# Optimization experiments

Hardware: AMD Instinct MI355X
Metric: run time of the kernel (lower is better)

## Reference

```python
import jax, jax.numpy as jnp
import numpy as np
import math

D_MODEL = 1024
NUM_HEADS = 16
B, L = 2, 2048
# scale_level=0, patch_time_span=1 -> effective_stride=1
PERIODS = (1.0, 30.0)
WEIGHTS = (0.8, 0.4)
SIGMAS = (0.5, 2.0)


def setup_inputs() -> dict:
    key = jax.random.key(0)
    ks = jax.random.split(key, 10)
    s = 1.0 / math.sqrt(D_MODEL)
    inp = {
        "x": jax.random.normal(ks[0], (B, L, D_MODEL), dtype=jnp.float32),
        "Wq": jax.random.normal(ks[1], (D_MODEL, D_MODEL), dtype=jnp.float32) * s,
        "bq": jax.random.normal(ks[2], (D_MODEL,), dtype=jnp.float32) * 0.01,
        "Wk": jax.random.normal(ks[3], (D_MODEL, D_MODEL), dtype=jnp.float32) * s,
        "bk": jax.random.normal(ks[4], (D_MODEL,), dtype=jnp.float32) * 0.01,
        "Wv": jax.random.normal(ks[5], (D_MODEL, D_MODEL), dtype=jnp.float32) * s,
        "bv": jax.random.normal(ks[6], (D_MODEL,), dtype=jnp.float32) * 0.01,
        "Wo": jax.random.normal(ks[7], (D_MODEL, D_MODEL), dtype=jnp.float32) * s,
        "bo": jax.random.normal(ks[8], (D_MODEL,), dtype=jnp.float32) * 0.01,
        "prior_lambda": jnp.asarray(2.0, dtype=jnp.float32),
    }
    return inp


def _gaussian_mask(length):
    idx = jnp.arange(length, dtype=jnp.float32)
    delta = jnp.abs(idx[:, None] - idx[None, :])  # [L, L]
    mask = jnp.zeros_like(delta)
    for p, w, sigma in zip(PERIODS, WEIGHTS, SIGMAS):
        if p < 0.2:
            continue
        mask = mask + w * jnp.exp(-((delta - p) ** 2) / (2.0 * sigma ** 2))
    return mask


def reference(x, Wq, bq, Wk, bk, Wv, bv, Wo, bo, prior_lambda):
    Bx, Lx, D = x.shape
    H = NUM_HEADS
    hd = D // H

    def split_heads(t):  # [B, L, D] -> [B, H, L, hd]
        return t.reshape(Bx, Lx, H, hd).transpose(0, 2, 1, 3)

    Q = split_heads(x @ Wq.T + bq)
    K = split_heads(x @ Wk.T + bk)
    V = split_heads(x @ Wv.T + bv)

    scores = jnp.einsum("bhqd,bhkd->bhqk", Q, K) / math.sqrt(hd)
    scores = scores + prior_lambda * _gaussian_mask(Lx)[None, None, :, :]
    attn = jax.nn.softmax(scores, axis=-1)
    out = jnp.einsum("bhqk,bhkd->bhqd", attn, V)
    out = out.transpose(0, 2, 1, 3).reshape(Bx, Lx, D)
    return out @ Wo.T + bo
```

## Files before the change

### kernel.cpp

```cpp
#include <hip/hip_runtime.h>

#define D_MODEL 1024
#define SEQ_L   2048
#define NHEADS  16
#define HDIM    64
#define NROWS   4096

typedef __attribute__((ext_vector_type(8))) short short8;
typedef __attribute__((ext_vector_type(4))) short short4v;
typedef __attribute__((ext_vector_type(4))) float floatx4;
typedef __attribute__((ext_vector_type(4))) unsigned short ushort4v;
typedef unsigned short ushort;

static __device__ __forceinline__ ushort f2bf(float f) {
    unsigned int u = __float_as_uint(f);
    u += 0x7FFFu + ((u >> 16) & 1u);
    return (ushort)(u >> 16);
}

static __device__ __forceinline__ floatx4 mfma16(short8 a, short8 b, floatx4 c) {
    return __builtin_amdgcn_mfma_f32_16x16x32_bf16(a, b, c, 0, 0, 0);
}

static __device__ __forceinline__ floatx4 mfma16k16(short4v a, short4v b, floatx4 c) {
    return __builtin_amdgcn_mfma_f32_16x16x16bf16_1k(a, b, c, 0, 0, 0);
}

static __device__ __forceinline__ void store8bf(ushort* dst, float4 a, float4 b) {
    uint4 pk;
    pk.x = (unsigned)f2bf(a.x) | ((unsigned)f2bf(a.y) << 16);
    pk.y = (unsigned)f2bf(a.z) | ((unsigned)f2bf(a.w) << 16);
    pk.z = (unsigned)f2bf(b.x) | ((unsigned)f2bf(b.y) << 16);
    pk.w = (unsigned)f2bf(b.z) | ((unsigned)f2bf(b.w) << 16);
    *(uint4*)dst = pk;
}

static __device__ __forceinline__ void gll16(const ushort* g, ushort* l) {
    __builtin_amdgcn_global_load_lds(
        (const __attribute__((address_space(1))) unsigned int*)(const unsigned int*)g,
        (__attribute__((address_space(3))) unsigned int*)(unsigned int*)l,
        16, 0, 0);
}

__global__ __launch_bounds__(256) void convert_bf16(
    const float* __restrict__ x,
    const float* __restrict__ wq, const float* __restrict__ wk,
    const float* __restrict__ wv, const float* __restrict__ wo,
    ushort* __restrict__ xb, ushort* __restrict__ wb3, ushort* __restrict__ wob)
{
    const int seg = blockIdx.y;
    const float* src;
    ushort* dst;
    int n;
    if      (seg == 0) { src = x;  dst = xb;                n = 4194304; }
    else if (seg == 1) { src = wq; dst = wb3;               n = 1048576; }
    else if (seg == 2) { src = wk; dst = wb3 + 1048576;     n = 1048576; }
    else if (seg == 3) { src = wv; dst = wb3 + 2097152;     n = 1048576; }
    else               { src = wo; dst = wob;               n = 1048576; }
    const int i = (blockIdx.x * 256 + threadIdx.x) * 8;
    if (i >= n) return;
    float4 a = *(const float4*)(src + i);
    float4 b = *(const float4*)(src + i + 4);
    store8bf(dst + i, a, b);
}

__global__ __launch_bounds__(256) void gemm_qkv(
    const ushort* __restrict__ A, const ushort* __restrict__ B,
    const float* __restrict__ bq, const float* __restrict__ bk,
    const float* __restrict__ bv,
    ushort* __restrict__ Qo, ushort* __restrict__ Ko, ushort* __restrict__ Vo)
{
    __shared__ ushort As[128 * 32];
    __shared__ ushort Bs[128 * 32];

    const int tid  = threadIdx.x;
    const int w    = tid >> 6;
    const int lane = tid & 63;
    const int l15  = lane & 15;
    const int quad = lane >> 4;
    const int wm   = w & 1;
    const int wn   = w >> 1;

    const int bm = blockIdx.y * 128;
    const int bn = blockIdx.x * 128;

    const int r0 = w * 16 + (lane >> 2);
    const int r1 = r0 + 64;
    const int c_ = lane & 3;
    const int g0 = c_ ^ ((r0 >> 1) & 3);
    const int g1 = c_ ^ ((r1 >> 1) & 3);

    const ushort* a0p = A + (size_t)(bm + r0) * 1024 + g0 * 8;
    const ushort* a1p = A + (size_t)(bm + r1) * 1024 + g1 * 8;
    const ushort* b0p = B + (size_t)(bn + r0) * 1024 + g0 * 8;
    const ushort* b1p = B + (size_t)(bn + r1) * 1024 + g1 * 8;
    ushort* lA0 = &As[r0 * 32 + c_ * 8];
    ushort* lA1 = &As[r1 * 32 + c_ * 8];
    ushort* lB0 = &Bs[r0 * 32 + c_ * 8];
    ushort* lB1 = &Bs[r1 * 32 + c_ * 8];

    const int cA = (quad ^ ((l15 >> 1) & 3)) * 8;

    floatx4 acc[4][4];
#pragma unroll
    for (int i = 0; i < 4; i++)
#pragma unroll
        for (int j = 0; j < 4; j++) acc[i][j] = (floatx4){0.f, 0.f, 0.f, 0.f};

    for (int k0 = 0; k0 < 1024; k0 += 32) {
        __syncthreads();
        gll16(a0p + k0, lA0);
        gll16(a1p + k0, lA1);
        gll16(b0p + k0, lB0);
        gll16(b1p + k0, lB1);
        __syncthreads();

        short8 af[4], bf[4];
#pragma unroll
        for (int mi = 0; mi < 4; mi++)
            af[mi] = *(const short8*)&As[(wm * 64 + mi * 16 + l15) * 32 + cA];
#pragma unroll
        for (int ni = 0; ni < 4; ni++)
            bf[ni] = *(const short8*)&Bs[(wn * 64 + ni * 16 + l15) * 32 + cA];
#pragma unroll
        for (int mi = 0; mi < 4; mi++)
#pragma unroll
            for (int ni = 0; ni < 4; ni++)
                acc[mi][ni] = mfma16(af[mi], bf[ni], acc[mi][ni]);
    }

#pragma unroll
    for (int ni = 0; ni < 4; ni++) {
        const int col = bn + wn * 64 + ni * 16 + l15;
        const int z = col >> 10;
        const int within = col & 1023;
        const int h  = within >> 6;
        const int hd = within & 63;
        const float* bias = (z == 0) ? bq : (z == 1) ? bk : bv;
        const float bvl = bias[within];
        if (z == 2) {
#pragma unroll
            for (int mi = 0; mi < 4; mi++) {
                const int row = bm + wm * 64 + mi * 16 + quad * 4;
                const int bb = row >> 11, li = row & 2047;
                ushort4v pk;
#pragma unroll
                for (int r = 0; r < 4; r++) pk[r] = f2bf(acc[mi][ni][r] + bvl);
                *(ushort4v*)(Vo + ((size_t)(bb * NHEADS + h) * HDIM + hd) * SEQ_L + li) = pk;
            }
        } else {
            const float scale = (z == 0) ? 0.125f : 1.0f;
            ushort* outp = (z == 0) ? Qo : Ko;
#pragma unroll
            for (int mi = 0; mi < 4; mi++) {
#pragma unroll
                for (int r = 0; r < 4; r++) {
                    const int row = bm + wm * 64 + mi * 16 + quad * 4 + r;
                    const int bb = row >> 11, li = row & 2047;
                    outp[((size_t)(bb * NHEADS + h) * SEQ_L + li) * HDIM + hd] =
                        f2bf((acc[mi][ni][r] + bvl) * scale);
                }
            }
        }
    }
}

__global__ __launch_bounds__(256) void attn(
    const ushort* __restrict__ Q,
    const ushort* __restrict__ K,
    const ushort* __restrict__ Vt,
    const float* __restrict__ lam,
    ushort* __restrict__ O)
{
    __shared__ float mtab[128];
    __shared__ ushort Ks[2][64 * 64];
    __shared__ ushort Vts[2][64 * 64];

    const int tid  = threadIdx.x;
    const int wave = tid >> 6;
    const int lane = tid & 63;
    const int l15  = lane & 15;
    const int quad = lane >> 4;

    const int qb = blockIdx.x;
    const int h  = blockIdx.y;
    const int bz = blockIdx.z;
    const int bh = bz * NHEADS + h;
    const int q0 = qb * 64;

    const float lambda = *lam;
    if (tid < 128) {
        float d  = (float)tid;
        float e1 = (d - 1.f) * (d - 1.f);
        float e2 = (d - 30.f) * (d - 30.f);
        mtab[tid] = lambda * (0.8f * __expf(-2.0f * e1) + 0.4f * __expf(-0.125f * e2));
    }

    const ushort* qp =
        Q + ((size_t)bh * SEQ_L + q0 + wave * 16 + l15) * HDIM + quad * 8;
    short8 qf[2];
    qf[0] = *(const short8*)qp;
    qf[1] = *(const short8*)(qp + 32);

    const ushort* kbase = K  + ((size_t)bh * SEQ_L) * HDIM;
    const ushort* vbase = Vt + ((size_t)bh * HDIM) * SEQ_L;

    const int cid0 = tid, cid1 = 256 + tid;
    const int row0 = cid0 >> 3, row1 = cid1 >> 3;
    const int cl0  = (cid0 & 7) ^ (row0 & 7);
    const int cl1  = (cid1 & 7) ^ (row1 & 7);
    const ushort* kg0 = kbase + (size_t)row0 * HDIM + cl0 * 8;
    const ushort* kg1 = kbase + (size_t)row1 * HDIM + cl1 * 8;
    const ushort* vg0 = vbase + (size_t)row0 * SEQ_L + cl0 * 8;
    const ushort* vg1 = vbase + (size_t)row1 * SEQ_L + cl1 * 8;

    floatx4 o[4];
#pragma unroll
    for (int i = 0; i < 4; i++) o[i] = (floatx4){0.f, 0.f, 0.f, 0.f};
    float lrun = 0.f;

    gll16(kg0, &Ks[0][cid0 * 8]);
    gll16(kg1, &Ks[0][cid1 * 8]);
    gll16(vg0, &Vts[0][cid0 * 8]);
    gll16(vg1, &Vts[0][cid1 * 8]);

    const int xo = l15 & 7;

    for (int j = 0; j < SEQ_L / 64; j++) {
        const int cur = j & 1;
        __syncthreads();
        if (j + 1 < SEQ_L / 64) {
            const int nxt = cur ^ 1;
            const int koff = (j + 1) * 64;
            gll16(kg0 + (size_t)koff * HDIM, &Ks[nxt][cid0 * 8]);
            gll16(kg1 + (size_t)koff * HDIM, &Ks[nxt][cid1 * 8]);
            gll16(vg0 + koff, &Vts[nxt][cid0 * 8]);
            gll16(vg1 + koff, &Vts[nxt][cid1 * 8]);
        }

        floatx4 s[4];
#pragma unroll
        for (int i = 0; i < 4; i++) s[i] = (floatx4){0.f, 0.f, 0.f, 0.f};
#pragma unroll
        for (int kk = 0; kk < 2; kk++) {
#pragma unroll
            for (int nt = 0; nt < 4; nt++) {
                const int slot = (kk * 4 + quad) ^ xo;
                short8 kf = *(const short8*)&Ks[cur][(nt * 16 + l15) * 64 + slot * 8];
                s[nt] = mfma16(kf, qf[kk], s[nt]);
            }
        }

        const int dj = j - qb;
        if (dj >= -1 && dj <= 1) {
            const int qg = q0 + wave * 16 + l15;
#pragma unroll
            for (int nt = 0; nt < 4; nt++) {
                const int kg = j * 64 + nt * 16 + quad * 4;
#pragma unroll
                for (int r = 0; r < 4; r++) {
                    int dq = qg - (kg + r);
                    int ad = dq < 0 ? -dq : dq;
                    s[nt][r] += mtab[ad];
                }
            }
        }

        short4v pb[4];
#pragma unroll
        for (int nt = 0; nt < 4; nt++) {
            unsigned ur[4];
#pragma unroll
            for (int r = 0; r < 4; r++) {
                float p = __expf(s[nt][r]);
                unsigned u = __float_as_uint(p);
                u += 0x7FFFu + ((u >> 16) & 1u);
                ur[r] = u;
                lrun += __uint_as_float(u & 0xFFFF0000u);
            }
            uint2 pk;
            pk.x = __builtin_amdgcn_perm(ur[1], ur[0], 0x07060302u);
            pk.y = __builtin_amdgcn_perm(ur[3], ur[2], 0x07060302u);
            pb[nt] = __builtin_bit_cast(short4v, pk);
        }

#pragma unroll
        for (int kc = 0; kc < 4; kc++) {
#pragma unroll
            for (int nt = 0; nt < 4; nt++) {
                const int slot = (2 * kc + (quad >> 1)) ^ xo;
                short4v vf = *(const short4v*)
                    &Vts[cur][(nt * 16 + l15) * 64 + slot * 8 + (quad & 1) * 4];
                o[nt] = mfma16k16(vf, pb[kc], o[nt]);
            }
        }
    }

    float s_ = lrun;
    s_ += __shfl_xor(s_, 16);
    s_ += __shfl_xor(s_, 32);
    const float linv = 1.f / s_;

    const int qg = q0 + wave * 16 + l15;
    ushort* obase = O + ((size_t)bz * SEQ_L + qg) * D_MODEL + h * HDIM;
#pragma unroll
    for (int nt = 0; nt < 4; nt++) {
        ushort4v pk;
#pragma unroll
        for (int r = 0; r < 4; r++) pk[r] = f2bf(o[nt][r] * linv);
        *(ushort4v*)(obase + nt * 16 + quad * 4) = pk;
    }
}

__global__ __launch_bounds__(256) void gemm_out(
    const ushort* __restrict__ A, const ushort* __restrict__ B,
    const float* __restrict__ bo, float* __restrict__ out)
{
    __shared__ ushort As[64 * 32];
    __shared__ ushort Bs[128 * 32];

    const int tid  = threadIdx.x;
    const int w    = tid >> 6;
    const int lane = tid & 63;
    const int l15  = lane & 15;
    const int quad = lane >> 4;

    const int bm = blockIdx.y * 64;
    const int bn = blockIdx.x * 128;

    const int r0 = w * 16 + (lane >> 2);
    const int r1 = r0 + 64;
    const int c_ = lane & 3;
    const int g0 = c_ ^ ((r0 >> 1) & 3);
    const int g1 = c_ ^ ((r1 >> 1) & 3);

    const ushort* a0p = A + (size_t)(bm + r0) * 1024 + g0 * 8;
    const ushort* b0p = B + (size_t)(bn + r0) * 1024 + g0 * 8;
    const ushort* b1p = B + (size_t)(bn + r1) * 1024 + g1 * 8;
    ushort* lA0 = &As[r0 * 32 + c_ * 8];
    ushort* lB0 = &Bs[r0 * 32 + c_ * 8];
    ushort* lB1 = &Bs[r1 * 32 + c_ * 8];

    const int cA = (quad ^ ((l15 >> 1) & 3)) * 8;

    floatx4 acc[4][2];
#pragma unroll
    for (int i = 0; i < 4; i++)
#pragma unroll
        for (int j = 0; j < 2; j++) acc[i][j] = (floatx4){0.f, 0.f, 0.f, 0.f};

    for (int k0 = 0; k0 < 1024; k0 += 32) {
        __syncthreads();
        gll16(a0p + k0, lA0);
        gll16(b0p + k0, lB0);
        gll16(b1p + k0, lB1);
        __syncthreads();

        short8 af[4], bf[2];
#pragma unroll
        for (int mi = 0; mi < 4; mi++)
            af[mi] = *(const short8*)&As[(mi * 16 + l15) * 32 + cA];
#pragma unroll
        for (int ni = 0; ni < 2; ni++)
            bf[ni] = *(const short8*)&Bs[(w * 32 + ni * 16 + l15) * 32 + cA];
#pragma unroll
        for (int mi = 0; mi < 4; mi++)
#pragma unroll
            for (int ni = 0; ni < 2; ni++)
                acc[mi][ni] = mfma16(af[mi], bf[ni], acc[mi][ni]);
    }

#pragma unroll
    for (int ni = 0; ni < 2; ni++) {
        const int col = bn + w * 32 + ni * 16 + l15;
        const float bvl = bo[col];
#pragma unroll
        for (int mi = 0; mi < 4; mi++) {
#pragma unroll
            for (int r = 0; r < 4; r++) {
                const int row = bm + mi * 16 + quad * 4 + r;
                out[(size_t)row * 1024 + col] = acc[mi][ni][r] + bvl;
            }
        }
    }
}

extern "C" void kernel_launch(void* const* d_in, const int* in_sizes, int n_in,
                              void* d_out, int out_size, void* d_ws, size_t ws_size,
                              hipStream_t stream)
{
    const float* x   = (const float*)d_in[0];
    const float* Wq  = (const float*)d_in[1];
    const float* bq  = (const float*)d_in[2];
    const float* Wk  = (const float*)d_in[3];
    const float* bk  = (const float*)d_in[4];
    const float* Wv  = (const float*)d_in[5];
    const float* bv  = (const float*)d_in[6];
    const float* Wo  = (const float*)d_in[7];
    const float* bo  = (const float*)d_in[8];
    const float* lam = (const float*)d_in[9];
    float* out = (float*)d_out;

    const size_t NELEM = (size_t)NROWS * D_MODEL;
    ushort* Qw  = (ushort*)d_ws;
    ushort* Kw  = Qw + NELEM;
    ushort* Vw  = Kw + NELEM;
    ushort* XA  = Vw + NELEM;
    ushort* Wb3 = XA + NELEM;
    ushort* Wob = Wb3 + 3 * 1024 * 1024;

    dim3 gc(2048, 5);
    convert_bf16<<<gc, 256, 0, stream>>>(x, Wq, Wk, Wv, Wo, XA, Wb3, Wob);

    dim3 g1(3072 / 128, NROWS / 128);
    gemm_qkv<<<g1, 256, 0, stream>>>(XA, Wb3, bq, bk, bv, Qw, Kw, Vw);

    dim3 g2(SEQ_L / 64, NHEADS, 2);
    attn<<<g2, 256, 0, stream>>>(Qw, Kw, Vw, lam, XA);

    dim3 g3(1024 / 128, NROWS / 64);
    gemm_out<<<g3, 256, 0, stream>>>(XA, Wob, bo, out);
}
```

Measured before the change: 224.4 us.

## Process two query tiles per attention block and use exp2 softmax

```diff
diff --git a/kernel.cpp b/kernel.cpp
--- a/kernel.cpp
+++ b/kernel.cpp
@@ -5,6 +5,15 @@
 #define NHEADS  16
 #define HDIM    64
 #define NROWS   4096
+
+#define QSCALE 0.18033688011112042f
+#define LOG2E  1.4426950408889634f
+
+#if __has_builtin(__builtin_amdgcn_exp2f)
+#define EXP2F(x) __builtin_amdgcn_exp2f(x)
+#else
+#define EXP2F(x) __expf((x) * 0.6931471805599453f)
+#endif
 
 typedef __attribute__((ext_vector_type(8))) short short8;
 typedef __attribute__((ext_vector_type(4))) short short4v;
@@ -149,7 +158,7 @@
                 *(ushort4v*)(Vo + ((size_t)(bb * NHEADS + h) * HDIM + hd) * SEQ_L + li) = pk;
             }
         } else {
-            const float scale = (z == 0) ? 0.125f : 1.0f;
+            const float scale = (z == 0) ? QSCALE : 1.0f;
             ushort* outp = (z == 0) ? Qo : Ko;
 #pragma unroll
             for (int mi = 0; mi < 4; mi++) {
@@ -186,21 +195,24 @@
     const int h  = blockIdx.y;
     const int bz = blockIdx.z;
     const int bh = bz * NHEADS + h;
-    const int q0 = qb * 64;
+    const int q0 = qb * 128;
 
     const float lambda = *lam;
     if (tid < 128) {
         float d  = (float)tid;
         float e1 = (d - 1.f) * (d - 1.f);
         float e2 = (d - 30.f) * (d - 30.f);
-        mtab[tid] = lambda * (0.8f * __expf(-2.0f * e1) + 0.4f * __expf(-0.125f * e2));
+        mtab[tid] = LOG2E * lambda *
+                    (0.8f * __expf(-2.0f * e1) + 0.4f * __expf(-0.125f * e2));
     }
 
     const ushort* qp =
         Q + ((size_t)bh * SEQ_L + q0 + wave * 16 + l15) * HDIM + quad * 8;
-    short8 qf[2];
-    qf[0] = *(const short8*)qp;
-    qf[1] = *(const short8*)(qp + 32);
+    short8 qf[2][2];
+    qf[0][0] = *(const short8*)qp;
+    qf[0][1] = *(const short8*)(qp + 32);
+    qf[1][0] = *(const short8*)(qp + 64 * HDIM);
+    qf[1][1] = *(const short8*)(qp + 64 * HDIM + 32);
 
     const ushort* kbase = K  + ((size_t)bh * SEQ_L) * HDIM;
     const ushort* vbase = Vt + ((size_t)bh * HDIM) * SEQ_L;
@@ -214,10 +226,12 @@
     const ushort* vg0 = vbase + (size_t)row0 * SEQ_L + cl0 * 8;
     const ushort* vg1 = vbase + (size_t)row1 * SEQ_L + cl1 * 8;
 
-    floatx4 o[4];
-#pragma unroll
-    for (int i = 0; i < 4; i++) o[i] = (floatx4){0.f, 0.f, 0.f, 0.f};
-    float lrun = 0.f;
+    floatx4 o[2][4];
+#pragma unroll
+    for (int g = 0; g < 2; g++)
+#pragma unroll
+        for (int i = 0; i < 4; i++) o[g][i] = (floatx4){0.f, 0.f, 0.f, 0.f};
+    float lrun[2] = {0.f, 0.f};
 
     gll16(kg0, &Ks[0][cid0 * 8]);
     gll16(kg1, &Ks[0][cid1 * 8]);
@@ -238,50 +252,57 @@
             gll16(vg1 + koff, &Vts[nxt][cid1 * 8]);
         }
 
-        floatx4 s[4];
-#pragma unroll
-        for (int i = 0; i < 4; i++) s[i] = (floatx4){0.f, 0.f, 0.f, 0.f};
+        floatx4 s[2][4];
+#pragma unroll
+        for (int g = 0; g < 2; g++)
+#pragma unroll
+            for (int i = 0; i < 4; i++) s[g][i] = (floatx4){0.f, 0.f, 0.f, 0.f};
 #pragma unroll
         for (int kk = 0; kk < 2; kk++) {
 #pragma unroll
             for (int nt = 0; nt < 4; nt++) {
                 const int slot = (kk * 4 + quad) ^ xo;
                 short8 kf = *(const short8*)&Ks[cur][(nt * 16 + l15) * 64 + slot * 8];
-                s[nt] = mfma16(kf, qf[kk], s[nt]);
-            }
-        }
-
-        const int dj = j - qb;
-        if (dj >= -1 && dj <= 1) {
-            const int qg = q0 + wave * 16 + l15;
+                s[0][nt] = mfma16(kf, qf[0][kk], s[0][nt]);
+                s[1][nt] = mfma16(kf, qf[1][kk], s[1][nt]);
+            }
+        }
+
+#pragma unroll
+        for (int g = 0; g < 2; g++) {
+            const int tg = j - (qb * 2 + g);
+            if (tg >= -1 && tg <= 1) {
+                const int qg = q0 + g * 64 + wave * 16 + l15;
+#pragma unroll
+                for (int nt = 0; nt < 4; nt++) {
+                    const int kg = j * 64 + nt * 16 + quad * 4;
+#pragma unroll
+                    for (int r = 0; r < 4; r++) {
+                        int dq = qg - (kg + r);
+                        int ad = dq < 0 ? -dq : dq;
+                        s[g][nt][r] += mtab[ad];
+                    }
+                }
+            }
+        }
+
+        short4v pb[2][4];
+#pragma unroll
+        for (int g = 0; g < 2; g++) {
 #pragma unroll
             for (int nt = 0; nt < 4; nt++) {
-                const int kg = j * 64 + nt * 16 + quad * 4;
+                unsigned ur[4];
 #pragma unroll
                 for (int r = 0; r < 4; r++) {
-                    int dq = qg - (kg + r);
-                    int ad = dq < 0 ? -dq : dq;
-                    s[nt][r] += mtab[ad];
+                    float p = EXP2F(s[g][nt][r]);
+                    lrun[g] += p;
+                    ur[r] = __float_as_uint(p) + 0x8000u;
                 }
-            }
-        }
-
-        short4v pb[4];
-#pragma unroll
-        for (int nt = 0; nt < 4; nt++) {
-            unsigned ur[4];
-#pragma unroll
-            for (int r = 0; r < 4; r++) {
-                float p = __expf(s[nt][r]);
-                unsigned u = __float_as_uint(p);
-                u += 0x7FFFu + ((u >> 16) & 1u);
-                ur[r] = u;
-                lrun += __uint_as_float(u & 0xFFFF0000u);
-            }
-            uint2 pk;
-            pk.x = __builtin_amdgcn_perm(ur[1], ur[0], 0x07060302u);
-            pk.y = __builtin_amdgcn_perm(ur[3], ur[2], 0x07060302u);
-            pb[nt] = __builtin_bit_cast(short4v, pk);
+                uint2 pk;
+                pk.x = __builtin_amdgcn_perm(ur[1], ur[0], 0x07060302u);
+                pk.y = __builtin_amdgcn_perm(ur[3], ur[2], 0x07060302u);
+                pb[g][nt] = __builtin_bit_cast(short4v, pk);
+            }
         }
 
 #pragma unroll
@@ -291,24 +312,27 @@
                 const int slot = (2 * kc + (quad >> 1)) ^ xo;
                 short4v vf = *(const short4v*)
                     &Vts[cur][(nt * 16 + l15) * 64 + slot * 8 + (quad & 1) * 4];
-                o[nt] = mfma16k16(vf, pb[kc], o[nt]);
-            }
-        }
-    }
-
-    float s_ = lrun;
-    s_ += __shfl_xor(s_, 16);
-    s_ += __shfl_xor(s_, 32);
-    const float linv = 1.f / s_;
-
-    const int qg = q0 + wave * 16 + l15;
-    ushort* obase = O + ((size_t)bz * SEQ_L + qg) * D_MODEL + h * HDIM;
-#pragma unroll
-    for (int nt = 0; nt < 4; nt++) {
-        ushort4v pk;
-#pragma unroll
-        for (int r = 0; r < 4; r++) pk[r] = f2bf(o[nt][r] * linv);
-        *(ushort4v*)(obase + nt * 16 + quad * 4) = pk;
+                o[0][nt] = mfma16k16(vf, pb[0][kc], o[0][nt]);
+                o[1][nt] = mfma16k16(vf, pb[1][kc], o[1][nt]);
+            }
+        }
+    }
+
+#pragma unroll
+    for (int g = 0; g < 2; g++) {
+        float s_ = lrun[g];
+        s_ += __shfl_xor(s_, 16);
+        s_ += __shfl_xor(s_, 32);
+        const float linv = 1.f / s_;
+        const int qg = q0 + g * 64 + wave * 16 + l15;
+        ushort* obase = O + ((size_t)bz * SEQ_L + qg) * D_MODEL + h * HDIM;
+#pragma unroll
+        for (int nt = 0; nt < 4; nt++) {
+            ushort4v pk;
+#pragma unroll
+            for (int r = 0; r < 4; r++) pk[r] = f2bf(o[g][nt][r] * linv);
+            *(ushort4v*)(obase + nt * 16 + quad * 4) = pk;
+        }
     }
 }
 
@@ -415,7 +439,7 @@
     dim3 g1(3072 / 128, NROWS / 128);
     gemm_qkv<<<g1, 256, 0, stream>>>(XA, Wb3, bq, bk, bv, Qw, Kw, Vw);
 
-    dim3 g2(SEQ_L / 64, NHEADS, 2);
+    dim3 g2(SEQ_L / 128, NHEADS, 2);
     attn<<<g2, 256, 0, stream>>>(Qw, Kw, Vw, lam, XA);
 
     dim3 g3(1024 / 128, NROWS / 64);
```

Result: faster. 217.0 us (-3.3%).
